# Optimization experiments

Measured on AMD Instinct MI355X. Metric: run time of the kernel, lower is better.

The kernel has to match this reference:

```python
import jax, jax.numpy as jnp
import numpy as np
import math

EMBED_DIM = 768
NUM_HEADS = 12
HEAD_DIM = EMBED_DIM // NUM_HEADS
B, T = 4, 2048
GATE_EPS = 1e-06


def setup_inputs() -> dict:
    key = jax.random.key(0)
    ks = jax.random.split(key, 10)
    s_in = 1.0 / math.sqrt(EMBED_DIM)   # fan-in init scale for D->hd projections
    s_hd = 1.0 / math.sqrt(HEAD_DIM)    # fan-in init scale for hd->D projection
    return {
        "hidden_states": jax.random.normal(ks[0], (B, T, EMBED_DIM), dtype=jnp.float32),
        "Wq": jax.random.normal(ks[1], (NUM_HEADS, EMBED_DIM, HEAD_DIM), dtype=jnp.float32) * s_in,
        "bq": jax.random.normal(ks[2], (NUM_HEADS, HEAD_DIM), dtype=jnp.float32) * s_in,
        "Wk": jax.random.normal(ks[3], (NUM_HEADS, EMBED_DIM, HEAD_DIM), dtype=jnp.float32) * s_in,
        "bk": jax.random.normal(ks[4], (NUM_HEADS, HEAD_DIM), dtype=jnp.float32) * s_in,
        "Wv": jax.random.normal(ks[5], (NUM_HEADS, EMBED_DIM, HEAD_DIM), dtype=jnp.float32) * s_in,
        "bv": jax.random.normal(ks[6], (NUM_HEADS, HEAD_DIM), dtype=jnp.float32) * s_in,
        "Wo": jax.random.normal(ks[7], (NUM_HEADS, HEAD_DIM, EMBED_DIM), dtype=jnp.float32) * s_hd,
        "bo": jax.random.normal(ks[8], (NUM_HEADS, EMBED_DIM), dtype=jnp.float32) * s_hd,
        "gate": jnp.ones((NUM_HEADS,), dtype=jnp.float32),
    }


def reference(hidden_states, Wq, bq, Wk, bk, Wv, bv, Wo, bo, gate):
    # Batched per-head QKV projections: btd,hde->bhte
    Q = jnp.einsum("btd,hde->bhte", hidden_states, Wq) + bq[None, :, None, :]
    K = jnp.einsum("btd,hde->bhte", hidden_states, Wk) + bk[None, :, None, :]
    V = jnp.einsum("btd,hde->bhte", hidden_states, Wv) + bv[None, :, None, :]
    scores = jnp.einsum("bhqe,bhke->bhqk", Q, K) / math.sqrt(HEAD_DIM)  # [B,H,T,T]
    weights = jax.nn.softmax(scores, axis=-1)
    attn = jnp.einsum("bhqk,bhke->bhqe", weights, V)  # [B,H,T,hd]
    # Per-head output projection (bias included), gated; zero out heads with gate < eps
    per_head = jnp.einsum("bhte,hed->bhtd", attn, Wo) + bo[None, :, None, :]
    g = jnp.where(gate < GATE_EPS, 0.0, gate)  # replicate host-side skip as mask
    out = jnp.einsum("bhtd,h->btd", per_head, g)  # gated sum over heads
    return out
```

## Files before the change

### kernel.cpp

```cpp
#include <hip/hip_runtime.h>
#include <math.h>

#define NH 12
#define DM 768
#define HD 64
#define BB 4
#define TT 2048
#define MTOT (BB*TT)

#define QSCALE 0.1803368801111204f

typedef short bf16x8 __attribute__((ext_vector_type(8)));
typedef short bf16x4 __attribute__((ext_vector_type(4)));
typedef float f32x4 __attribute__((ext_vector_type(4)));
typedef int   i32x4 __attribute__((ext_vector_type(4)));
typedef int   i32x2 __attribute__((ext_vector_type(2)));
typedef unsigned int u32;

#define GLDS(g, l) __builtin_amdgcn_global_load_lds((const __attribute__((address_space(1))) u32*)(g), (__attribute__((address_space(3))) u32*)(l), 16, 0, 0)

__device__ __forceinline__ unsigned short f2bf(float f) {
    unsigned u = __float_as_uint(f);
    u += 0x7fff + ((u >> 16) & 1);
    return (unsigned short)(u >> 16);
}

__global__ void k_pack_x(const float* __restrict__ x, unsigned short* __restrict__ xb) {
    int i = (blockIdx.x * blockDim.x + threadIdx.x) * 4;
    float4 v = *(const float4*)(x + i);
    ushort4 o = { f2bf(v.x), f2bf(v.y), f2bf(v.z), f2bf(v.w) };
    *(ushort4*)(xb + i) = o;
}

__global__ void k_pack_wqkv(const float* __restrict__ Wq, const float* __restrict__ Wk,
                            const float* __restrict__ Wv, unsigned short* __restrict__ wt) {
    __shared__ unsigned short L[64][72];
    const int bid = blockIdx.x;
    const int q = bid / 144, r = bid % 144, h = r / 12, kt = r % 12;
    const float* W = (q == 0 ? Wq : (q == 1 ? Wk : Wv)) + (size_t)h * DM * HD + (size_t)kt * 64 * HD;
    #pragma unroll
    for (int it = 0; it < 4; it++) {
        int idx = it * 256 + threadIdx.x;
        int rr = idx >> 4, e4 = (idx & 15) * 4;
        float4 v = *(const float4*)&W[(size_t)rr * HD + e4];
        L[e4    ][rr] = f2bf(v.x);
        L[e4 + 1][rr] = f2bf(v.y);
        L[e4 + 2][rr] = f2bf(v.z);
        L[e4 + 3][rr] = f2bf(v.w);
    }
    __syncthreads();
    #pragma unroll
    for (int it = 0; it < 2; it++) {
        int idx = it * 256 + threadIdx.x;
        int e = idx >> 3, c8 = (idx & 7) * 8;
        *(bf16x8*)&wt[(size_t)(q * 768 + h * 64 + e) * DM + kt * 64 + c8] = *(const bf16x8*)&L[e][c8];
    }
}

__global__ void k_pack_wo(const float* __restrict__ Wo, const float* __restrict__ gate,
                          unsigned short* __restrict__ wt) {
    __shared__ unsigned short L[64][72];
    const int bid = blockIdx.x;
    const int ht = bid / 12, dt = bid % 12;
    float g = gate[ht]; g = (g < 1e-6f) ? 0.f : g;
    const float* W = Wo + (size_t)ht * 64 * DM + dt * 64;
    #pragma unroll
    for (int it = 0; it < 4; it++) {
        int idx = it * 256 + threadIdx.x;
        int rr = idx >> 4, d4 = (idx & 15) * 4;
        float4 v = *(const float4*)&W[(size_t)rr * DM + d4];
        L[d4    ][rr] = f2bf(g * v.x);
        L[d4 + 1][rr] = f2bf(g * v.y);
        L[d4 + 2][rr] = f2bf(g * v.z);
        L[d4 + 3][rr] = f2bf(g * v.w);
    }
    __syncthreads();
    #pragma unroll
    for (int it = 0; it < 2; it++) {
        int idx = it * 256 + threadIdx.x;
        int d = idx >> 3, c8 = (idx & 7) * 8;
        *(bf16x8*)&wt[(size_t)(dt * 64 + d) * DM + ht * 64 + c8] = *(const bf16x8*)&L[d][c8];
    }
}

__global__ void k_bias_o(const float* __restrict__ bo, const float* __restrict__ gate,
                         float* __restrict__ bias) {
    int d = blockIdx.x * blockDim.x + threadIdx.x;
    if (d < DM) {
        float s = 0.f;
        #pragma unroll
        for (int h = 0; h < NH; h++) {
            float g = gate[h]; g = (g < 1e-6f) ? 0.f : g;
            s += g * bo[h * DM + d];
        }
        bias[d] = s;
    }
}

__global__ __launch_bounds__(256) void k_gemm_qkv(
    const unsigned short* __restrict__ A,
    const unsigned short* __restrict__ Bt,
    const float* __restrict__ bq, const float* __restrict__ bk, const float* __restrict__ bv,
    unsigned short* __restrict__ Q, unsigned short* __restrict__ Kg, unsigned short* __restrict__ Vt)
{
    __shared__ unsigned short As[2][4096];
    __shared__ unsigned short Bs[2][4096];
    const int flat = blockIdx.y * 18 + blockIdx.x;
    const int swz  = (flat & 7) * 144 + (flat >> 3);
    const int m0 = (swz / 18) * 128, n0 = (swz % 18) * 128;
    const int tid = threadIdx.x, lane = tid & 63, w = tid >> 6;
    const int wr = (w >> 1) * 64, wc = (w & 1) * 64;
    const int lr = lane & 15, lq = lane >> 4;

    const int arow = tid >> 2;
    const int ag   = ((tid & 3) ^ (arow & 3)) * 8;
    const int ldsw = w * 512;
    const int kg = (lq ^ (lr & 3)) * 8;

    #define STAGE_G(k0_, buf_) do { \
        const unsigned short* a_ = A  + (size_t)(m0 + arow) * DM + (k0_) + ag; \
        const unsigned short* b_ = Bt + (size_t)(n0 + arow) * DM + (k0_) + ag; \
        GLDS(a_,             &As[buf_][ldsw]); \
        GLDS(a_ + 64 * DM,   &As[buf_][2048 + ldsw]); \
        GLDS(b_,             &Bs[buf_][ldsw]); \
        GLDS(b_ + 64 * DM,   &Bs[buf_][2048 + ldsw]); \
    } while (0)

    f32x4 acc[4][4] = {};
    STAGE_G(0, 0);
    for (int it = 0; it < DM / 32; it++) {
        const int cur = it & 1;
        __syncthreads();
        if (it < DM / 32 - 1) STAGE_G((it + 1) * 32, cur ^ 1);
        bf16x8 af[4], bf[4];
        #pragma unroll
        for (int rt = 0; rt < 4; rt++) af[rt] = *(const bf16x8*)&As[cur][(wr + rt*16 + lr) * 32 + kg];
        #pragma unroll
        for (int ct = 0; ct < 4; ct++) bf[ct] = *(const bf16x8*)&Bs[cur][(wc + ct*16 + lr) * 32 + kg];
        #pragma unroll
        for (int rt = 0; rt < 4; rt++)
            #pragma unroll
            for (int ct = 0; ct < 4; ct++)
                acc[rt][ct] = __builtin_amdgcn_mfma_f32_16x16x32_bf16(af[rt], bf[ct], acc[rt][ct], 0, 0, 0);
    }
    #undef STAGE_G

    const int region = n0 / DM;
    const int b  = m0 >> 11;
    const int tb = m0 & 2047;
    if (region == 2) {
        #pragma unroll
        for (int rt = 0; rt < 4; rt++)
          #pragma unroll
          for (int ct = 0; ct < 4; ct++) {
            int n = n0 + wc + ct*16 + lr, r = n - 2*DM;
            int h = r >> 6, e = r & 63;
            int t0 = tb + wr + rt*16 + lq*4;
            float bias = bv[r];
            ushort4 o;
            o.x = f2bf(acc[rt][ct][0] + bias);
            o.y = f2bf(acc[rt][ct][1] + bias);
            o.z = f2bf(acc[rt][ct][2] + bias);
            o.w = f2bf(acc[rt][ct][3] + bias);
            *(ushort4*)&Vt[((size_t)(b*NH + h)*HD + e)*TT + t0] = o;
          }
    } else {
        const float* bias_p = (region == 0) ? bq : bk;
        const float  scale  = (region == 0) ? QSCALE : 1.0f;
        unsigned short* dst = (region == 0) ? Q : Kg;
        #pragma unroll
        for (int rt = 0; rt < 4; rt++)
          #pragma unroll
          for (int ct = 0; ct < 4; ct++) {
            int n = n0 + wc + ct*16 + lr, r = n - region*DM;
            int h = r >> 6, e = r & 63;
            float bias = bias_p[r];
            #pragma unroll
            for (int i = 0; i < 4; i++) {
                int t = tb + wr + rt*16 + lq*4 + i;
                dst[((size_t)(b*NH + h)*TT + t)*HD + e] = f2bf((acc[rt][ct][i] + bias) * scale);
            }
          }
    }
}

__global__ __launch_bounds__(256) void k_flash(
    const unsigned short* __restrict__ Q, const unsigned short* __restrict__ Kg,
    const unsigned short* __restrict__ Vt, unsigned short* __restrict__ A2)
{
    __shared__ unsigned short Ks[2][4096];
    __shared__ unsigned short Vs[2][4096];
    const int flat = blockIdx.y * (BB*NH) + blockIdx.x;
    const int swz  = (flat & 7) * 96 + (flat >> 3);
    const int bh = swz >> 4, qt = swz & 15;
    const int b = bh / NH, h = bh % NH;
    const int tid = threadIdx.x, lane = tid & 63, w = tid >> 6;
    const int col = lane & 15, quad = lane >> 4;
    const size_t qk_base = (size_t)bh * TT * HD;
    const size_t vt_base = (size_t)bh * HD * TT;
    const int tq0 = qt * 128 + w * 32;

    const int srow  = tid >> 3;
    const int sperm = (tid & 7) ^ (srow & 7);
    const int koff0 = srow * HD + sperm * 8;
    const int voff0 = srow * TT + sperm * 8;
    const int lds0  = w * 512;

    const unsigned short* ksrc = Kg + qk_base;
    const unsigned short* vsrc = Vt + vt_base;

    const int c7 = col & 7;
    const int ra0 = col * 64 + (((    quad) ^ c7) * 8);
    const int ra1 = col * 64 + (((4 + quad) ^ c7) * 8);
    const int q2 = quad >> 1, q1 = (quad & 1) * 4;

    bf16x8 aq[2][2];
    #pragma unroll
    for (int rt = 0; rt < 2; rt++)
        #pragma unroll
        for (int ks = 0; ks < 2; ks++)
            aq[rt][ks] = *(const bf16x8*)&Q[qk_base + (size_t)(tq0 + rt*16 + col) * HD + ks*32 + quad*8];

    const bf16x4 ones4 = { (short)0x3F80, (short)0x3F80, (short)0x3F80, (short)0x3F80 };

    f32x4 co[4][2] = {};
    f32x4 lacc[2] = {};

    #define STAGE(kt_, buf_) do { \
        const unsigned short* kb_ = ksrc + (size_t)(kt_) * 64 * HD; \
        const unsigned short* vb_ = vsrc + (kt_) * 64; \
        GLDS(kb_ + koff0,           &Ks[buf_][lds0]); \
        GLDS(kb_ + koff0 + 32*HD,   &Ks[buf_][lds0 + 2048]); \
        GLDS(vb_ + voff0,           &Vs[buf_][lds0]); \
        GLDS(vb_ + voff0 + 32*TT,   &Vs[buf_][lds0 + 2048]); \
    } while (0)

    STAGE(0, 0);

    for (int kt = 0; kt < TT/64; kt++) {
        const int cur = kt & 1;
        __syncthreads();
        if (kt < TT/64 - 1) STAGE(kt + 1, cur ^ 1);

        bf16x8 kf[4][2];
        #pragma unroll
        for (int ct = 0; ct < 4; ct++) {
            kf[ct][0] = *(const bf16x8*)&Ks[cur][ct*1024 + ra0];
            kf[ct][1] = *(const bf16x8*)&Ks[cur][ct*1024 + ra1];
        }

        f32x4 cs[4][2] = {};
        __builtin_amdgcn_s_setprio(1);
        #pragma unroll
        for (int ks = 0; ks < 2; ks++)
            #pragma unroll
            for (int ct = 0; ct < 4; ct++)
                #pragma unroll
                for (int rt = 0; rt < 2; rt++)
                    cs[ct][rt] = __builtin_amdgcn_mfma_f32_16x16x32_bf16(kf[ct][ks], aq[rt][ks], cs[ct][rt], 0, 0, 0);
        __builtin_amdgcn_s_setprio(0);

        int pk[2][4][2];
        #pragma unroll
        for (int rt = 0; rt < 2; rt++) {
            #pragma unroll
            for (int ct = 0; ct < 4; ct++) {
                float p0 = __builtin_amdgcn_exp2f(cs[ct][rt][0]);
                float p1 = __builtin_amdgcn_exp2f(cs[ct][rt][1]);
                float p2 = __builtin_amdgcn_exp2f(cs[ct][rt][2]);
                float p3 = __builtin_amdgcn_exp2f(cs[ct][rt][3]);
                pk[rt][ct][0] = (int)__builtin_amdgcn_perm(__float_as_uint(p1), __float_as_uint(p0), 0x07060302u);
                pk[rt][ct][1] = (int)__builtin_amdgcn_perm(__float_as_uint(p3), __float_as_uint(p2), 0x07060302u);
            }
        }

        __builtin_amdgcn_s_setprio(1);
        #pragma unroll
        for (int ct = 0; ct < 4; ct++) {
            bf16x4 pb[2];
            #pragma unroll
            for (int rt = 0; rt < 2; rt++) {
                i32x2 t2; t2[0] = pk[rt][ct][0]; t2[1] = pk[rt][ct][1];
                pb[rt] = __builtin_bit_cast(bf16x4, t2);
                lacc[rt] = __builtin_amdgcn_mfma_f32_16x16x16bf16_1k(ones4, pb[rt], lacc[rt], 0, 0, 0);
            }
            const int va = ((ct*2 + q2) ^ c7) * 8 + q1;
            #pragma unroll
            for (int cv = 0; cv < 4; cv++) {
                bf16x4 vf4 = *(const bf16x4*)&Vs[cur][cv*1024 + col*64 + va];
                #pragma unroll
                for (int rt = 0; rt < 2; rt++)
                    co[cv][rt] = __builtin_amdgcn_mfma_f32_16x16x16bf16_1k(vf4, pb[rt], co[cv][rt], 0, 0, 0);
            }
        }
        __builtin_amdgcn_s_setprio(0);
    }
    #undef STAGE

    #pragma unroll
    for (int rt = 0; rt < 2; rt++) {
        float inv = 1.0f / lacc[rt][0];
        int t = tq0 + rt*16 + col;
        #pragma unroll
        for (int cv = 0; cv < 4; cv++) {
            ushort4 o;
            o.x = f2bf(co[cv][rt][0] * inv);
            o.y = f2bf(co[cv][rt][1] * inv);
            o.z = f2bf(co[cv][rt][2] * inv);
            o.w = f2bf(co[cv][rt][3] * inv);
            *(ushort4*)&A2[(size_t)(b*TT + t) * DM + h*HD + cv*16 + quad*4] = o;
        }
    }
}

__global__ __launch_bounds__(256) void k_gemm_out(
    const unsigned short* __restrict__ A,
    const unsigned short* __restrict__ Bt,
    const float* __restrict__ bias,
    float* __restrict__ out)
{
    __shared__ unsigned short As[2][4096];
    __shared__ unsigned short Bs[2][4096];
    const int flat = blockIdx.y * 6 + blockIdx.x;
    const int swz  = (flat & 7) * 48 + (flat >> 3);
    const int m0 = (swz / 6) * 128, n0 = (swz % 6) * 128;
    const int tid = threadIdx.x, lane = tid & 63, w = tid >> 6;
    const int wr = (w >> 1) * 64, wc = (w & 1) * 64;
    const int lr = lane & 15, lq = lane >> 4;

    const int arow = tid >> 2;
    const int ag   = ((tid & 3) ^ (arow & 3)) * 8;
    const int ldsw = w * 512;
    const int kg = (lq ^ (lr & 3)) * 8;

    #define STAGE_G(k0_, buf_) do { \
        const unsigned short* a_ = A  + (size_t)(m0 + arow) * DM + (k0_) + ag; \
        const unsigned short* b_ = Bt + (size_t)(n0 + arow) * DM + (k0_) + ag; \
        GLDS(a_,             &As[buf_][ldsw]); \
        GLDS(a_ + 64 * DM,   &As[buf_][2048 + ldsw]); \
        GLDS(b_,             &Bs[buf_][ldsw]); \
        GLDS(b_ + 64 * DM,   &Bs[buf_][2048 + ldsw]); \
    } while (0)

    f32x4 acc[4][4] = {};
    STAGE_G(0, 0);
    for (int it = 0; it < DM / 32; it++) {
        const int cur = it & 1;
        __syncthreads();
        if (it < DM / 32 - 1) STAGE_G((it + 1) * 32, cur ^ 1);
        bf16x8 af[4], bf[4];
        #pragma unroll
        for (int rt = 0; rt < 4; rt++) af[rt] = *(const bf16x8*)&As[cur][(wr + rt*16 + lr) * 32 + kg];
        #pragma unroll
        for (int ct = 0; ct < 4; ct++) bf[ct] = *(const bf16x8*)&Bs[cur][(wc + ct*16 + lr) * 32 + kg];
        #pragma unroll
        for (int rt = 0; rt < 4; rt++)
            #pragma unroll
            for (int ct = 0; ct < 4; ct++)
                acc[rt][ct] = __builtin_amdgcn_mfma_f32_16x16x32_bf16(af[rt], bf[ct], acc[rt][ct], 0, 0, 0);
    }
    #undef STAGE_G

    #pragma unroll
    for (int rt = 0; rt < 4; rt++)
      #pragma unroll
      for (int ct = 0; ct < 4; ct++)
        #pragma unroll
        for (int i = 0; i < 4; i++) {
            int m = m0 + wr + rt*16 + lq*4 + i;
            int n = n0 + wc + ct*16 + lr;
            out[(size_t)m * DM + n] = acc[rt][ct][i] + bias[n];
        }
}

extern "C" void kernel_launch(void* const* d_in, const int* in_sizes, int n_in,
                              void* d_out, int out_size, void* d_ws, size_t ws_size,
                              hipStream_t stream) {
    const float* x    = (const float*)d_in[0];
    const float* Wq   = (const float*)d_in[1];
    const float* bq   = (const float*)d_in[2];
    const float* Wk   = (const float*)d_in[3];
    const float* bk   = (const float*)d_in[4];
    const float* Wv   = (const float*)d_in[5];
    const float* bv   = (const float*)d_in[6];
    const float* Wo   = (const float*)d_in[7];
    const float* bo   = (const float*)d_in[8];
    const float* gate = (const float*)d_in[9];
    float* out = (float*)d_out;

    char* p = (char*)d_ws;
    unsigned short* Xb   = (unsigned short*)p;  p += (size_t)MTOT*DM*2;
    unsigned short* Wqkv = (unsigned short*)p;  p += (size_t)3*DM*DM*2;
    unsigned short* Qb   = (unsigned short*)p;  p += (size_t)BB*NH*TT*HD*2;
    unsigned short* Kb   = (unsigned short*)p;  p += (size_t)BB*NH*TT*HD*2;
    unsigned short* Vtb  = (unsigned short*)p;  p += (size_t)BB*NH*TT*HD*2;
    unsigned short* A2   = (unsigned short*)p;  p += (size_t)MTOT*DM*2;
    unsigned short* Wob  = (unsigned short*)p;  p += (size_t)DM*DM*2;
    float*          bio  = (float*)p;           p += (size_t)DM*4;

    k_pack_x   <<<(MTOT*DM/4 + 255)/256, 256, 0, stream>>>(x, Xb);
    k_pack_wqkv<<<3*12*12, 256, 0, stream>>>(Wq, Wk, Wv, Wqkv);
    k_pack_wo  <<<12*12, 256, 0, stream>>>(Wo, gate, Wob);
    k_bias_o   <<<3, 256, 0, stream>>>(bo, gate, bio);
    k_gemm_qkv <<<dim3((3*DM)/128, MTOT/128), 256, 0, stream>>>(Xb, Wqkv, bq, bk, bv, Qb, Kb, Vtb);
    k_flash    <<<dim3(BB*NH, TT/128), 256, 0, stream>>>(Qb, Kb, Vtb, A2);
    k_gemm_out <<<dim3(DM/128, MTOT/128), 256, 0, stream>>>(A2, Wob, bio, out);
}
```

Before: 274.7 us.

## Stage P through LDS to use 16x16x32 MFMA for PV and row sums

Result: faster. 245.0 us (-10.8%).

```diff
diff --git a/kernel.cpp b/kernel.cpp
--- a/kernel.cpp
+++ b/kernel.cpp
@@ -184,12 +184,13 @@
     }
 }
 
-__global__ __launch_bounds__(256) void k_flash(
+__global__ __launch_bounds__(256, 3) void k_flash(
     const unsigned short* __restrict__ Q, const unsigned short* __restrict__ Kg,
     const unsigned short* __restrict__ Vt, unsigned short* __restrict__ A2)
 {
     __shared__ unsigned short Ks[2][4096];
     __shared__ unsigned short Vs[2][4096];
+    __shared__ unsigned short Ps[4][32][72];
     const int flat = blockIdx.y * (BB*NH) + blockIdx.x;
     const int swz  = (flat & 7) * 96 + (flat >> 3);
     const int bh = swz >> 4, qt = swz & 15;
@@ -212,7 +213,6 @@
     const int c7 = col & 7;
     const int ra0 = col * 64 + (((    quad) ^ c7) * 8);
     const int ra1 = col * 64 + (((4 + quad) ^ c7) * 8);
-    const int q2 = quad >> 1, q1 = (quad & 1) * 4;
 
     bf16x8 aq[2][2];
     #pragma unroll
@@ -221,7 +221,8 @@
         for (int ks = 0; ks < 2; ks++)
             aq[rt][ks] = *(const bf16x8*)&Q[qk_base + (size_t)(tq0 + rt*16 + col) * HD + ks*32 + quad*8];
 
-    const bf16x4 ones4 = { (short)0x3F80, (short)0x3F80, (short)0x3F80, (short)0x3F80 };
+    const bf16x8 ones8 = { (short)0x3F80, (short)0x3F80, (short)0x3F80, (short)0x3F80,
+                           (short)0x3F80, (short)0x3F80, (short)0x3F80, (short)0x3F80 };
 
     f32x4 co[4][2] = {};
     f32x4 lacc[2] = {};
@@ -274,23 +275,34 @@
             }
         }
 
+        #pragma unroll
+        for (int rt = 0; rt < 2; rt++)
+            #pragma unroll
+            for (int ct = 0; ct < 4; ct++) {
+                i32x2 t2; t2[0] = pk[rt][ct][0]; t2[1] = pk[rt][ct][1];
+                *(i32x2*)&Ps[w][rt*16 + col][ct*16 + quad*4] = t2;
+            }
+        bf16x8 pf[2][2];
+        #pragma unroll
+        for (int rt = 0; rt < 2; rt++)
+            #pragma unroll
+            for (int k4 = 0; k4 < 2; k4++)
+                pf[rt][k4] = *(const bf16x8*)&Ps[w][rt*16 + col][k4*32 + quad*8];
+
         __builtin_amdgcn_s_setprio(1);
         #pragma unroll
-        for (int ct = 0; ct < 4; ct++) {
-            bf16x4 pb[2];
-            #pragma unroll
-            for (int rt = 0; rt < 2; rt++) {
-                i32x2 t2; t2[0] = pk[rt][ct][0]; t2[1] = pk[rt][ct][1];
-                pb[rt] = __builtin_bit_cast(bf16x4, t2);
-                lacc[rt] = __builtin_amdgcn_mfma_f32_16x16x16bf16_1k(ones4, pb[rt], lacc[rt], 0, 0, 0);
-            }
-            const int va = ((ct*2 + q2) ^ c7) * 8 + q1;
-            #pragma unroll
-            for (int cv = 0; cv < 4; cv++) {
-                bf16x4 vf4 = *(const bf16x4*)&Vs[cur][cv*1024 + col*64 + va];
+        for (int rt = 0; rt < 2; rt++)
+            #pragma unroll
+            for (int k4 = 0; k4 < 2; k4++)
+                lacc[rt] = __builtin_amdgcn_mfma_f32_16x16x32_bf16(ones8, pf[rt][k4], lacc[rt], 0, 0, 0);
+        #pragma unroll
+        for (int cv = 0; cv < 4; cv++) {
+            #pragma unroll
+            for (int k4 = 0; k4 < 2; k4++) {
+                bf16x8 vf = *(const bf16x8*)&Vs[cur][cv*1024 + col*64 + ((k4*4 + quad) ^ c7)*8];
                 #pragma unroll
                 for (int rt = 0; rt < 2; rt++)
-                    co[cv][rt] = __builtin_amdgcn_mfma_f32_16x16x16bf16_1k(vf4, pb[rt], co[cv][rt], 0, 0, 0);
+                    co[cv][rt] = __builtin_amdgcn_mfma_f32_16x16x32_bf16(vf, pf[rt][k4], co[cv][rt], 0, 0, 0);
             }
         }
         __builtin_amdgcn_s_setprio(0);
```
